# Optimization experiments

Hardware: AMD Instinct MI355X
Metric: run time of the kernel (lower is better)

Reference implementation:

```python
import jax, jax.numpy as jnp
import numpy as np
import math

B, C, L = 16, 2048, 64

def setup_inputs() -> dict:
    key = jax.random.key(0)
    kq, kk, kv = jax.random.split(key, 3)
    q = jax.random.normal(kq, (B, C, L), dtype=jnp.float32)
    k = jax.random.normal(kk, (B, C, L), dtype=jnp.float32)
    v = jax.random.normal(kv, (B, C, L), dtype=jnp.float32)
    return {"q": q, "k": k, "v": v}

def reference(q, k, v):
    b, c, l = q.shape
    # Faithful to the torch source: k is RESHAPED (row-major), not transposed.
    k_t = k.reshape(b, l, c)                      # (b, l, c)
    score = jnp.matmul(q, k_t) / math.sqrt(l)     # (b, c, c)
    # nn.Softmax() with no dim on a 3D tensor -> torch implicit dim = 0 (batch axis)
    score = jax.nn.softmax(score, axis=0)
    return jnp.matmul(score, v)                   # (b, c, l)
```

## Files before the change

### kernel.cpp

```cpp
#include <hip/hip_runtime.h>

typedef __attribute__((ext_vector_type(8))) short short8;
typedef __attribute__((ext_vector_type(4))) float float4v;

#define BATCH 16
#define CDIM 2048
#define LDIM 64
#define BSTRIDE (CDIM * LDIM)

#if __has_builtin(__builtin_amdgcn_exp2f)
#define EXPW(x) __builtin_amdgcn_exp2f(x)
#define QSCALE 0.18033688011112042f
#else
#define EXPW(x) __expf(x)
#define QSCALE 0.125f
#endif

__device__ __forceinline__ float bf2f(unsigned short u) {
    return __uint_as_float(((unsigned int)u) << 16);
}
__device__ __forceinline__ unsigned short f2bf(float f) {
    unsigned int x = __float_as_uint(f);
    x += 0x7fffu + ((x >> 16) & 1u);
    return (unsigned short)(x >> 16);
}
#if __has_builtin(__builtin_amdgcn_cvt_pk_bf16_f32)
__device__ __forceinline__ unsigned int pk2bf(float a, float b) {
    auto t = __builtin_amdgcn_cvt_pk_bf16_f32(a, b);
    unsigned int u;
    __builtin_memcpy(&u, &t, 4);
    return u;
}
#else
__device__ __forceinline__ unsigned int pk2bf(float a, float b) {
    return f2bf(a) | ((unsigned)f2bf(b) << 16);
}
#endif
__device__ __forceinline__ void dma16(const void* g, void* l) {
    __builtin_amdgcn_global_load_lds(
        (const __attribute__((address_space(1))) void*)g,
        (__attribute__((address_space(3))) void*)l, 16, 0, 0);
}

__global__ __launch_bounds__(256) void prepass_kernel(
    const float* __restrict__ q, const float* __restrict__ k,
    unsigned short* __restrict__ qb, unsigned short* __restrict__ kT)
{
    __shared__ float T[64][68];
    const int bx = blockIdx.x;
    const int t = threadIdx.x;

    if (bx < 1024) {
        int i = bx * 256 + t;
        const float4v* src = (const float4v*)q + (size_t)i * 2;
        float4v x0 = src[0], x1 = src[1];
        unsigned int u0 = pk2bf(x0[0] * QSCALE, x0[1] * QSCALE);
        unsigned int u1 = pk2bf(x0[2] * QSCALE, x0[3] * QSCALE);
        unsigned int u2 = pk2bf(x1[0] * QSCALE, x1[1] * QSCALE);
        unsigned int u3 = pk2bf(x1[2] * QSCALE, x1[3] * QSCALE);
        int b = i >> 14, r = i & 16383, m = r >> 3, j = r & 7;
        *(uint4*)(qb + (size_t)b * BSTRIDE + m * 64 + (j ^ (m & 7)) * 8) =
            make_uint4(u0, u1, u2, u3);
    } else {
        int idx = bx - 1024, b = idx >> 5, n0 = (idx & 31) * 64;
        const float* src = k + (size_t)b * BSTRIDE + (size_t)(t >> 2) * 2048 + n0 + (t & 3) * 16;
#pragma unroll
        for (int kk = 0; kk < 4; kk++) {
            float4v x = *(const float4v*)(src + kk * 4);
#pragma unroll
            for (int e = 0; e < 4; e++)
                T[t >> 2][(t & 3) * 16 + kk * 4 + e] = x[e];
        }
        __syncthreads();
        unsigned short* dst = kT + (size_t)b * BSTRIDE;
        int n = t & 63;
#pragma unroll
        for (int jj = 0; jj < 2; jj++) {
            int j = (t >> 6) * 2 + jj;
            *(uint4*)(dst + (size_t)(n0 + n) * 64 + (j ^ (n & 7)) * 8) =
                make_uint4(pk2bf(T[j * 8 + 0][n], T[j * 8 + 1][n]),
                           pk2bf(T[j * 8 + 2][n], T[j * 8 + 3][n]),
                           pk2bf(T[j * 8 + 4][n], T[j * 8 + 5][n]),
                           pk2bf(T[j * 8 + 6][n], T[j * 8 + 7][n]));
        }
    }
}

__global__ __launch_bounds__(256, 3) void dinv_vpre_kernel(
    const unsigned short* __restrict__ qb, const unsigned short* __restrict__ kT,
    const float* __restrict__ v, unsigned short* __restrict__ vS,
    unsigned short* __restrict__ Dt)
{
    __shared__ __align__(16) unsigned char smem[17408];

    const int tid = threadIdx.x;

    if (blockIdx.x >= 512) {
        float (*T)[68] = (float(*)[68])smem;
#pragma unroll 1
        for (int tt = 0; tt < 2; tt++) {
            int idx = (blockIdx.x - 512) * 2 + tt, b = idx >> 5, n0 = (idx & 31) * 64;
            const float* src = v + (size_t)b * BSTRIDE + (size_t)n0 * 64 +
                               (size_t)(tid >> 2) * 64 + (tid & 3) * 16;
#pragma unroll
            for (int kk = 0; kk < 4; kk++) {
                float4v x = *(const float4v*)(src + kk * 4);
#pragma unroll
                for (int e = 0; e < 4; e++)
                    T[tid >> 2][(tid & 3) * 16 + kk * 4 + e] = x[e];
            }
            __syncthreads();
            unsigned short* dst = vS + (size_t)b * BSTRIDE;
            int j = tid & 63, qc = tid >> 6;
            int sw = qc ^ (j & 3) ^ ((j >> 2) & 3);
#pragma unroll
            for (int nb = 0; nb < 2; nb++) {
                *(uint4*)(dst + (size_t)(n0 / 32 + nb) * 2048 + j * 32 + sw * 8) =
                    make_uint4(pk2bf(T[nb * 32 + qc * 8 + 0][j], T[nb * 32 + qc * 8 + 1][j]),
                               pk2bf(T[nb * 32 + qc * 8 + 2][j], T[nb * 32 + qc * 8 + 3][j]),
                               pk2bf(T[nb * 32 + qc * 8 + 4][j], T[nb * 32 + qc * 8 + 5][j]),
                               pk2bf(T[nb * 32 + qc * 8 + 6][j], T[nb * 32 + qc * 8 + 7][j]));
            }
            __syncthreads();
        }
        return;
    }

    const int w = tid >> 6, lane = tid & 63;
    const int c = lane & 15, q = lane >> 4;
    const int xcd = blockIdx.x & 7, slot = blockIdx.x >> 3;
    const int mtB = xcd * 2 + (slot >> 5), ng = slot & 31;
    const int m0 = mtB * 128, n0 = ng * 64;

    float4v Dacc[2][4];
#pragma unroll
    for (int ms = 0; ms < 2; ms++)
#pragma unroll
        for (int nt = 0; nt < 4; nt++) Dacc[ms][nt] = (float4v){0.f, 0.f, 0.f, 0.f};

    const char* qrow0 = (const char*)qb + (size_t)(m0 + w * 32 + c) * 128;
    short8 Qf[2][2], Qn[2][2];
#pragma unroll
    for (int ms = 0; ms < 2; ms++)
#pragma unroll
        for (int h = 0; h < 2; h++)
            Qf[ms][h] = *(const short8*)(qrow0 + ms * 16 * 128 + ((h * 4 + q) ^ (c & 7)) * 16);

    {
        const char* kg = (const char*)(kT + (size_t)n0 * 64);
        dma16(kg + (w * 2 + 0) * 1024 + lane * 16, (char*)smem + (w * 2 + 0) * 1024);
        dma16(kg + (w * 2 + 1) * 1024 + lane * 16, (char*)smem + (w * 2 + 1) * 1024);
    }

    for (int bb = 0; bb < BATCH; bb++) {
        const int p = bb & 1;
        asm volatile("s_waitcnt vmcnt(0)" ::: "memory");
        asm volatile("s_barrier" ::: "memory");
        if (bb < BATCH - 1) {
            const char* kg = (const char*)(kT + (size_t)(bb + 1) * BSTRIDE + (size_t)n0 * 64);
            dma16(kg + (w * 2 + 0) * 1024 + lane * 16,
                  (char*)smem + (p ^ 1) * 8192 + (w * 2 + 0) * 1024);
            dma16(kg + (w * 2 + 1) * 1024 + lane * 16,
                  (char*)smem + (p ^ 1) * 8192 + (w * 2 + 1) * 1024);
            const char* qn = qrow0 + (size_t)(bb + 1) * (BSTRIDE * 2);
#pragma unroll
            for (int ms = 0; ms < 2; ms++)
#pragma unroll
                for (int h = 0; h < 2; h++)
                    Qn[ms][h] = *(const short8*)(qn + ms * 16 * 128 + ((h * 4 + q) ^ (c & 7)) * 16);
        }
        const char* sk = (const char*)smem + p * 8192;
#pragma unroll
        for (int nt = 0; nt < 4; nt++) {
            short8 A0 = *(const short8*)(sk + (nt * 16 + c) * 128 + ((q) ^ (c & 7)) * 16);
            short8 A1 = *(const short8*)(sk + (nt * 16 + c) * 128 + ((4 + q) ^ (c & 7)) * 16);
#pragma unroll
            for (int ms = 0; ms < 2; ms++) {
                float4v d = (float4v){0.f, 0.f, 0.f, 0.f};
                d = __builtin_amdgcn_mfma_f32_16x16x32_bf16(A0, Qf[ms][0], d, 0, 0, 0);
                d = __builtin_amdgcn_mfma_f32_16x16x32_bf16(A1, Qf[ms][1], d, 0, 0, 0);
#pragma unroll
                for (int r = 0; r < 4; r++) Dacc[ms][nt][r] += EXPW(d[r]);
            }
        }
        if (bb < BATCH - 1) {
#pragma unroll
            for (int ms = 0; ms < 2; ms++)
#pragma unroll
                for (int h = 0; h < 2; h++)
                    Qf[ms][h] = Qn[ms][h];
        }
    }

#pragma unroll
    for (int ms = 0; ms < 2; ms++)
#pragma unroll
        for (int nt = 0; nt < 4; nt++) {
            unsigned int x = pk2bf(__builtin_amdgcn_rcpf(Dacc[ms][nt][0]),
                                   __builtin_amdgcn_rcpf(Dacc[ms][nt][1]));
            unsigned int y = pk2bf(__builtin_amdgcn_rcpf(Dacc[ms][nt][2]),
                                   __builtin_amdgcn_rcpf(Dacc[ms][nt][3]));
            size_t tm = (size_t)(mtB * 8 + w * 2 + ms);
            size_t tp = (size_t)(ng * 2 + (nt >> 1));
            *(uint2*)((char*)Dt + (tm * 64 + tp) * 1024 + c * 64 + q * 16 + (nt & 1) * 8) =
                make_uint2(x, y);
        }
}

__global__ __launch_bounds__(512, 4) void attn_main_kernel(
    const unsigned short* __restrict__ qb, const unsigned short* __restrict__ kT,
    const unsigned short* __restrict__ vS, const unsigned short* __restrict__ Dt,
    float* __restrict__ out)
{
    __shared__ __align__(16) unsigned char smem[36864];

    const int tid = threadIdx.x, w = tid >> 6, lane = tid & 63;
    const int c = lane & 15, q = lane >> 4;
    const int g = w >> 2, ns = w & 3;
    const int xcd = blockIdx.x & 7, slot = blockIdx.x >> 3;
    const int b = slot & 15, mt = xcd * 4 + (slot >> 4);
    const int m0 = mt * 64;
    const int nbase = ns * 512;

    const unsigned short* qb_b = qb + (size_t)b * BSTRIDE;
    const char* kbase = (const char*)(kT + (size_t)b * BSTRIDE);
    const char* vbase = (const char*)(vS + (size_t)b * BSTRIDE);
    char* skb = (char*)smem + ns * 8192;

    short8 Qf[2][2];
#pragma unroll
    for (int ms = 0; ms < 2; ms++)
#pragma unroll
        for (int h = 0; h < 2; h++)
            Qf[ms][h] = *(const short8*)(qb_b + (m0 + g * 32 + ms * 16 + c) * 64 +
                                         ((h * 4 + q) ^ (c & 7)) * 8);
    float4v acc[2][4];
#pragma unroll
    for (int ms = 0; ms < 2; ms++)
#pragma unroll
        for (int jt = 0; jt < 4; jt++) acc[ms][jt] = (float4v){0.f, 0.f, 0.f, 0.f};

    const char* dtw0 = (const char*)Dt +
        ((size_t)(mt * 4 + g * 2 + 0) * 64 + ns * 16) * 1024 + c * 64 + q * 16;
    const char* dtw1 = dtw0 + (size_t)64 * 1024;

    const int vsw = (q ^ (c & 3) ^ ((c >> 2) & 3)) * 16;

    dma16(kbase + (size_t)nbase * 128 + (2 * g + 0) * 1024 + lane * 16, skb + (2 * g + 0) * 1024);
    dma16(kbase + (size_t)nbase * 128 + (2 * g + 1) * 1024 + lane * 16, skb + (2 * g + 1) * 1024);
    uint4 du[2];
    du[0] = *(const uint4*)(dtw0);
    du[1] = *(const uint4*)(dtw1);

    for (int st = 0; st < 16; st++) {
        const int p = st & 1;
        asm volatile("s_waitcnt vmcnt(0)" ::: "memory");
        asm volatile("s_barrier" ::: "memory");

        uint4 nu[2] = {du[0], du[1]};
        if (st < 15) {
            const int n1 = nbase + (st + 1) * 32;
            dma16(kbase + (size_t)n1 * 128 + (2 * g + 0) * 1024 + lane * 16,
                  skb + (p ^ 1) * 4096 + (2 * g + 0) * 1024);
            dma16(kbase + (size_t)n1 * 128 + (2 * g + 1) * 1024 + lane * 16,
                  skb + (p ^ 1) * 4096 + (2 * g + 1) * 1024);
            nu[0] = *(const uint4*)(dtw0 + (size_t)(st + 1) * 1024);
            nu[1] = *(const uint4*)(dtw1 + (size_t)(st + 1) * 1024);
        }

        short8 Vr[4];
        {
            const char* vtile = vbase + (size_t)(ns * 16 + st) * 4096;
#pragma unroll
            for (int jt = 0; jt < 4; jt++)
                Vr[jt] = *(const short8*)(vtile + (jt * 16 + c) * 64 + vsw);
        }

        const char* skp = skb + p * 4096;
        unsigned int pr[2][2][2];
#pragma unroll
        for (int nt = 0; nt < 2; nt++) {
            short8 A0 = *(const short8*)(skp + (nt * 16 + c) * 128 + ((q) ^ (c & 7)) * 16);
            short8 A1 = *(const short8*)(skp + (nt * 16 + c) * 128 + ((4 + q) ^ (c & 7)) * 16);
#pragma unroll
            for (int ms = 0; ms < 2; ms++) {
                float4v d = (float4v){0.f, 0.f, 0.f, 0.f};
                d = __builtin_amdgcn_mfma_f32_16x16x32_bf16(A0, Qf[ms][0], d, 0, 0, 0);
                d = __builtin_amdgcn_mfma_f32_16x16x32_bf16(A1, Qf[ms][1], d, 0, 0, 0);
                unsigned int ux = nt ? du[ms].z : du[ms].x;
                unsigned int uy = nt ? du[ms].w : du[ms].y;
                pr[ms][nt][0] = pk2bf(EXPW(d[0]) * __uint_as_float(ux << 16),
                                      EXPW(d[1]) * __uint_as_float(ux & 0xffff0000u));
                pr[ms][nt][1] = pk2bf(EXPW(d[2]) * __uint_as_float(uy << 16),
                                      EXPW(d[3]) * __uint_as_float(uy & 0xffff0000u));
            }
        }

        union PU { unsigned int i[4]; short8 s; };
        PU pu0, pu1;
#if __has_builtin(__builtin_amdgcn_permlane32_swap) && __has_builtin(__builtin_amdgcn_permlane16_swap)
        {
            typedef __attribute__((ext_vector_type(2))) unsigned int uint2v;
            uint2v ab, cd;
            ab = __builtin_amdgcn_permlane32_swap(pr[0][0][0], pr[0][1][0], false, false);
            cd = __builtin_amdgcn_permlane16_swap(ab.x, ab.y, false, false);
            pu0.i[0] = cd.x; pu0.i[2] = cd.y;
            ab = __builtin_amdgcn_permlane32_swap(pr[0][0][1], pr[0][1][1], false, false);
            cd = __builtin_amdgcn_permlane16_swap(ab.x, ab.y, false, false);
            pu0.i[1] = cd.x; pu0.i[3] = cd.y;
            ab = __builtin_amdgcn_permlane32_swap(pr[1][0][0], pr[1][1][0], false, false);
            cd = __builtin_amdgcn_permlane16_swap(ab.x, ab.y, false, false);
            pu1.i[0] = cd.x; pu1.i[2] = cd.y;
            ab = __builtin_amdgcn_permlane32_swap(pr[1][0][1], pr[1][1][1], false, false);
            cd = __builtin_amdgcn_permlane16_swap(ab.x, ab.y, false, false);
            pu1.i[1] = cd.x; pu1.i[3] = cd.y;
        }
#else
#pragma unroll
        for (int t = 0; t < 4; t++) {
            int src = (2 * (q & 1) + (t >> 1)) * 16 + c;
            int a0 = __shfl((int)pr[0][0][t & 1], src);
            int b0 = __shfl((int)pr[0][1][t & 1], src);
            pu0.i[t] = (unsigned int)((q >= 2) ? b0 : a0);
            int a1 = __shfl((int)pr[1][0][t & 1], src);
            int b1 = __shfl((int)pr[1][1][t & 1], src);
            pu1.i[t] = (unsigned int)((q >= 2) ? b1 : a1);
        }
#endif

#pragma unroll
        for (int jt = 0; jt < 4; jt++) {
            acc[0][jt] = __builtin_amdgcn_mfma_f32_16x16x32_bf16(pu0.s, Vr[jt], acc[0][jt], 0, 0, 0);
            acc[1][jt] = __builtin_amdgcn_mfma_f32_16x16x32_bf16(pu1.s, Vr[jt], acc[1][jt], 0, 0, 0);
        }
        du[0] = nu[0]; du[1] = nu[1];
    }

    __syncthreads();
    {
        float* cpy = (float*)((char*)smem + (ns & 1) * 17408);
        if (ns < 2) {
#pragma unroll
            for (int ms = 0; ms < 2; ms++)
#pragma unroll
                for (int jt = 0; jt < 4; jt++)
#pragma unroll
                    for (int r = 0; r < 4; r++)
                        cpy[(g * 32 + ms * 16 + q * 4 + r) * 68 + jt * 16 + c] = acc[ms][jt][r];
        }
    }
    __syncthreads();
    {
        float* cpy = (float*)((char*)smem + (ns & 1) * 17408);
        if (ns >= 2) {
#pragma unroll
            for (int ms = 0; ms < 2; ms++)
#pragma unroll
                for (int jt = 0; jt < 4; jt++)
#pragma unroll
                    for (int r = 0; r < 4; r++)
                        cpy[(g * 32 + ms * 16 + q * 4 + r) * 68 + jt * 16 + c] += acc[ms][jt][r];
        }
    }
    __syncthreads();
    {
        int ml = tid >> 3, j0 = (tid & 7) * 8;
        const float* c0 = (const float*)smem + ml * 68 + j0;
        const float* c1 = (const float*)((char*)smem + 17408) + ml * 68 + j0;
        float4v s0 = *(const float4v*)c0 + *(const float4v*)c1;
        float4v s1 = *(const float4v*)(c0 + 4) + *(const float4v*)(c1 + 4);
        float* dst = out + ((size_t)b * CDIM + m0 + ml) * LDIM + j0;
        *(float4v*)dst = s0;
        *(float4v*)(dst + 4) = s1;
    }
}

extern "C" void kernel_launch(void* const* d_in, const int* in_sizes, int n_in,
                              void* d_out, int out_size, void* d_ws, size_t ws_size,
                              hipStream_t stream) {
    const float* q = (const float*)d_in[0];
    const float* k = (const float*)d_in[1];
    const float* v = (const float*)d_in[2];
    float* out = (float*)d_out;

    unsigned short* qb = (unsigned short*)d_ws;
    unsigned short* kT = qb + (size_t)BATCH * BSTRIDE;
    unsigned short* vS = kT + (size_t)BATCH * BSTRIDE;
    unsigned short* Dt = vS + (size_t)BATCH * BSTRIDE;

    prepass_kernel<<<1536, 256, 0, stream>>>(q, k, qb, kT);
    dinv_vpre_kernel<<<768, 256, 0, stream>>>(qb, kT, v, vS, Dt);
    attn_main_kernel<<<512, 512, 0, stream>>>(qb, kT, vS, Dt, out);
}
```

Baseline: 121.7 us.

## Triple-buffer K tiles with two-ahead prefetch and partial vmcnt waits

Both kernels move from double-buffered to triple-buffered LDS for the K tiles. Each tile is now prefetched two iterations ahead, and the full vmcnt(0) drain is replaced by partial waits, so global loads overlap more compute. The MFMA/exp regions are also wrapped in s_setprio to favour matrix work. The cost is more LDS per block (24KB and 48KB), which could reduce occupancy, and the hand-counted vmcnt values must match the actual number of outstanding loads or results will be wrong.

After: 118.6 us (median of 2 runs). -2.6%, faster.

```diff
diff --git a/kernel.cpp b/kernel.cpp
--- a/kernel.cpp
+++ b/kernel.cpp
@@ -15,6 +15,9 @@
 #define EXPW(x) __expf(x)
 #define QSCALE 0.125f
 #endif
+
+#define WAITV(n) asm volatile("s_waitcnt vmcnt(" #n ")" ::: "memory")
+#define BARRIER() asm volatile("s_barrier" ::: "memory")
 
 __device__ __forceinline__ float bf2f(unsigned short u) {
     return __uint_as_float(((unsigned int)u) << 16);
@@ -91,7 +94,7 @@
     const float* __restrict__ v, unsigned short* __restrict__ vS,
     unsigned short* __restrict__ Dt)
 {
-    __shared__ __align__(16) unsigned char smem[17408];
+    __shared__ __align__(16) unsigned char smem[24576];
 
     const int tid = threadIdx.x;
 
@@ -147,21 +150,22 @@
             Qf[ms][h] = *(const short8*)(qrow0 + ms * 16 * 128 + ((h * 4 + q) ^ (c & 7)) * 16);
 
     {
-        const char* kg = (const char*)(kT + (size_t)n0 * 64);
-        dma16(kg + (w * 2 + 0) * 1024 + lane * 16, (char*)smem + (w * 2 + 0) * 1024);
-        dma16(kg + (w * 2 + 1) * 1024 + lane * 16, (char*)smem + (w * 2 + 1) * 1024);
-    }
-
+        const char* kg0 = (const char*)(kT + (size_t)n0 * 64);
+        const char* kg1 = (const char*)(kT + (size_t)BSTRIDE + (size_t)n0 * 64);
+        dma16(kg0 + (w * 2 + 0) * 1024 + lane * 16, (char*)smem + (w * 2 + 0) * 1024);
+        dma16(kg0 + (w * 2 + 1) * 1024 + lane * 16, (char*)smem + (w * 2 + 1) * 1024);
+        dma16(kg1 + (w * 2 + 0) * 1024 + lane * 16, (char*)smem + 8192 + (w * 2 + 0) * 1024);
+        dma16(kg1 + (w * 2 + 1) * 1024 + lane * 16, (char*)smem + 8192 + (w * 2 + 1) * 1024);
+    }
+
+    int cur = 0, pre = 2;
     for (int bb = 0; bb < BATCH; bb++) {
-        const int p = bb & 1;
-        asm volatile("s_waitcnt vmcnt(0)" ::: "memory");
-        asm volatile("s_barrier" ::: "memory");
+        if (bb == 0) { WAITV(2); }
+        else if (bb == 15) { WAITV(4); }
+        else { WAITV(6); }
+        BARRIER();
+
         if (bb < BATCH - 1) {
-            const char* kg = (const char*)(kT + (size_t)(bb + 1) * BSTRIDE + (size_t)n0 * 64);
-            dma16(kg + (w * 2 + 0) * 1024 + lane * 16,
-                  (char*)smem + (p ^ 1) * 8192 + (w * 2 + 0) * 1024);
-            dma16(kg + (w * 2 + 1) * 1024 + lane * 16,
-                  (char*)smem + (p ^ 1) * 8192 + (w * 2 + 1) * 1024);
             const char* qn = qrow0 + (size_t)(bb + 1) * (BSTRIDE * 2);
 #pragma unroll
             for (int ms = 0; ms < 2; ms++)
@@ -169,7 +173,15 @@
                 for (int h = 0; h < 2; h++)
                     Qn[ms][h] = *(const short8*)(qn + ms * 16 * 128 + ((h * 4 + q) ^ (c & 7)) * 16);
         }
-        const char* sk = (const char*)smem + p * 8192;
+        if (bb < BATCH - 2) {
+            const char* kg = (const char*)(kT + (size_t)(bb + 2) * BSTRIDE + (size_t)n0 * 64);
+            dma16(kg + (w * 2 + 0) * 1024 + lane * 16,
+                  (char*)smem + pre * 8192 + (w * 2 + 0) * 1024);
+            dma16(kg + (w * 2 + 1) * 1024 + lane * 16,
+                  (char*)smem + pre * 8192 + (w * 2 + 1) * 1024);
+        }
+        const char* sk = (const char*)smem + cur * 8192;
+        __builtin_amdgcn_s_setprio(1);
 #pragma unroll
         for (int nt = 0; nt < 4; nt++) {
             short8 A0 = *(const short8*)(sk + (nt * 16 + c) * 128 + ((q) ^ (c & 7)) * 16);
@@ -183,6 +195,7 @@
                 for (int r = 0; r < 4; r++) Dacc[ms][nt][r] += EXPW(d[r]);
             }
         }
+        __builtin_amdgcn_s_setprio(0);
         if (bb < BATCH - 1) {
 #pragma unroll
             for (int ms = 0; ms < 2; ms++)
@@ -190,6 +203,8 @@
                 for (int h = 0; h < 2; h++)
                     Qf[ms][h] = Qn[ms][h];
         }
+        cur = (cur == 2) ? 0 : cur + 1;
+        pre = (pre == 2) ? 0 : pre + 1;
     }
 
 #pragma unroll
@@ -212,7 +227,7 @@
     const unsigned short* __restrict__ vS, const unsigned short* __restrict__ Dt,
     float* __restrict__ out)
 {
-    __shared__ __align__(16) unsigned char smem[36864];
+    __shared__ __align__(16) unsigned char smem[49152];
 
     const int tid = threadIdx.x, w = tid >> 6, lane = tid & 63;
     const int c = lane & 15, q = lane >> 4;
@@ -225,7 +240,7 @@
     const unsigned short* qb_b = qb + (size_t)b * BSTRIDE;
     const char* kbase = (const char*)(kT + (size_t)b * BSTRIDE);
     const char* vbase = (const char*)(vS + (size_t)b * BSTRIDE);
-    char* skb = (char*)smem + ns * 8192;
+    char* skb = (char*)smem + ns * 12288;
 
     short8 Qf[2][2];
 #pragma unroll
@@ -248,26 +263,26 @@
 
     dma16(kbase + (size_t)nbase * 128 + (2 * g + 0) * 1024 + lane * 16, skb + (2 * g + 0) * 1024);
     dma16(kbase + (size_t)nbase * 128 + (2 * g + 1) * 1024 + lane * 16, skb + (2 * g + 1) * 1024);
+    dma16(kbase + (size_t)(nbase + 32) * 128 + (2 * g + 0) * 1024 + lane * 16,
+          skb + 4096 + (2 * g + 0) * 1024);
+    dma16(kbase + (size_t)(nbase + 32) * 128 + (2 * g + 1) * 1024 + lane * 16,
+          skb + 4096 + (2 * g + 1) * 1024);
     uint4 du[2];
     du[0] = *(const uint4*)(dtw0);
     du[1] = *(const uint4*)(dtw1);
 
+    int cur = 0, pre = 2;
     for (int st = 0; st < 16; st++) {
-        const int p = st & 1;
-        asm volatile("s_waitcnt vmcnt(0)" ::: "memory");
-        asm volatile("s_barrier" ::: "memory");
+        if (st == 0) { WAITV(4); }
+        else if (st == 15) { WAITV(0); }
+        else { WAITV(8); }
+        BARRIER();
 
         uint4 nu[2] = {du[0], du[1]};
         if (st < 15) {
-            const int n1 = nbase + (st + 1) * 32;
-            dma16(kbase + (size_t)n1 * 128 + (2 * g + 0) * 1024 + lane * 16,
-                  skb + (p ^ 1) * 4096 + (2 * g + 0) * 1024);
-            dma16(kbase + (size_t)n1 * 128 + (2 * g + 1) * 1024 + lane * 16,
-                  skb + (p ^ 1) * 4096 + (2 * g + 1) * 1024);
             nu[0] = *(const uint4*)(dtw0 + (size_t)(st + 1) * 1024);
             nu[1] = *(const uint4*)(dtw1 + (size_t)(st + 1) * 1024);
         }
-
         short8 Vr[4];
         {
             const char* vtile = vbase + (size_t)(ns * 16 + st) * 4096;
@@ -275,9 +290,17 @@
             for (int jt = 0; jt < 4; jt++)
                 Vr[jt] = *(const short8*)(vtile + (jt * 16 + c) * 64 + vsw);
         }
-
-        const char* skp = skb + p * 4096;
+        if (st < 14) {
+            const int n2 = nbase + (st + 2) * 32;
+            dma16(kbase + (size_t)n2 * 128 + (2 * g + 0) * 1024 + lane * 16,
+                  skb + pre * 4096 + (2 * g + 0) * 1024);
+            dma16(kbase + (size_t)n2 * 128 + (2 * g + 1) * 1024 + lane * 16,
+                  skb + pre * 4096 + (2 * g + 1) * 1024);
+        }
+
+        const char* skp = skb + cur * 4096;
         unsigned int pr[2][2][2];
+        __builtin_amdgcn_s_setprio(1);
 #pragma unroll
         for (int nt = 0; nt < 2; nt++) {
             short8 A0 = *(const short8*)(skp + (nt * 16 + c) * 128 + ((q) ^ (c & 7)) * 16);
@@ -295,6 +318,7 @@
                                       EXPW(d[3]) * __uint_as_float(uy & 0xffff0000u));
             }
         }
+        __builtin_amdgcn_s_setprio(0);
 
         union PU { unsigned int i[4]; short8 s; };
         PU pu0, pu1;
@@ -328,12 +352,16 @@
         }
 #endif
 
+        __builtin_amdgcn_s_setprio(1);
 #pragma unroll
         for (int jt = 0; jt < 4; jt++) {
             acc[0][jt] = __builtin_amdgcn_mfma_f32_16x16x32_bf16(pu0.s, Vr[jt], acc[0][jt], 0, 0, 0);
             acc[1][jt] = __builtin_amdgcn_mfma_f32_16x16x32_bf16(pu1.s, Vr[jt], acc[1][jt], 0, 0, 0);
         }
+        __builtin_amdgcn_s_setprio(0);
         du[0] = nu[0]; du[1] = nu[1];
+        cur = (cur == 2) ? 0 : cur + 1;
+        pre = (pre == 2) ? 0 : pre + 1;
     }
 
     __syncthreads();
```
